# Kernel tuning notes

Hardware: AMD Instinct MI355X
Metric: run time of the kernel (lower is better)

Reference implementation:

```python
import jax, jax.numpy as jnp
import numpy as np
import math

D_MODEL, N_HEADS, D_HEAD = 1024, 16, 64
INIT_RANGE = 0.02
IGNORE = -100000.0


def setup_inputs() -> dict:
    key = jax.random.key(0)
    ks = jax.random.split(key, 5)
    x = jax.random.normal(ks[0], (2, 2048, D_MODEL), dtype=jnp.float32)
    W_Q = INIT_RANGE * jax.random.normal(ks[1], (N_HEADS, D_MODEL, D_HEAD), dtype=jnp.float32)
    W_K = INIT_RANGE * jax.random.normal(ks[2], (N_HEADS, D_MODEL, D_HEAD), dtype=jnp.float32)
    W_V = INIT_RANGE * jax.random.normal(ks[3], (N_HEADS, D_MODEL, D_HEAD), dtype=jnp.float32)
    # W_O is contracted as 'n_heads d_head d_model' in the original einsum
    W_O = INIT_RANGE * jax.random.normal(ks[4], (N_HEADS, D_HEAD, D_MODEL), dtype=jnp.float32)
    b_Q = jnp.zeros((N_HEADS, D_HEAD), dtype=jnp.float32)
    b_K = jnp.zeros((N_HEADS, D_HEAD), dtype=jnp.float32)
    b_V = jnp.zeros((N_HEADS, D_HEAD), dtype=jnp.float32)
    b_O = jnp.zeros((D_MODEL,), dtype=jnp.float32)
    return {"normalized_resid_pre": x, "W_Q": W_Q, "b_Q": b_Q, "W_K": W_K, "b_K": b_K,
            "W_V": W_V, "b_V": b_V, "W_O": W_O, "b_O": b_O}


def reference(normalized_resid_pre, W_Q, b_Q, W_K, b_K, W_V, b_V, W_O, b_O):
    x = normalized_resid_pre  # [b, s, d_model]
    q = jnp.einsum('bsd,hde->bshe', x, W_Q) + b_Q  # [b, s, h, d_head]
    k = jnp.einsum('bsd,hde->bshe', x, W_K) + b_K
    v = jnp.einsum('bsd,hde->bshe', x, W_V) + b_V
    scores = jnp.einsum('bqhe,bkhe->bhqk', q, k) / math.sqrt(D_HEAD)
    S = x.shape[1]
    causal = jnp.tril(jnp.ones((S, S), dtype=bool))  # True where allowed
    scores = jnp.where(causal, scores, IGNORE)
    pattern = jax.nn.softmax(scores, axis=-1)  # [b, h, q, k]
    z = jnp.einsum('bhqk,bkhe->bqhe', pattern, v)
    attn_out = jnp.einsum('bqhe,hed->bqd', z, W_O) + b_O
    return attn_out
```

## Files before the change

### kernel.cpp

```cpp
#include <hip/hip_runtime.h>
#include <cstdint>
#include <cstddef>

typedef unsigned short u16;
typedef __bf16 bf16x8 __attribute__((ext_vector_type(8)));
typedef _Float16 f16x4 __attribute__((ext_vector_type(4)));
typedef _Float16 f16x2 __attribute__((ext_vector_type(2)));
typedef float  f32x4  __attribute__((ext_vector_type(4)));
typedef unsigned short u16x8 __attribute__((ext_vector_type(8)));
typedef unsigned short u16x4 __attribute__((ext_vector_type(4)));

#define DM   1024
#define NH   16
#define DH   64
#define SS   2048
#define BSZ  4096
#define NQKV 3072
#define QSCALE 0.18033688011f

__device__ __forceinline__ u16 f2b(float f) {
  unsigned u = __builtin_bit_cast(unsigned, f);
  return (u16)((u + 0x7FFFu + ((u >> 16) & 1u)) >> 16);
}
__device__ __forceinline__ u16 f2h(float f) {
  _Float16 h = (_Float16)f;
  return __builtin_bit_cast(u16, h);
}

__device__ __forceinline__ void gl_lds16(const void* g, void* l) {
  __builtin_amdgcn_global_load_lds(
      (__attribute__((address_space(1))) void*)(void*)g,
      (__attribute__((address_space(3))) void*)l, 16, 0, 0);
}

__global__ __launch_bounds__(256) void prep_all_kernel(
    const float* __restrict__ x, u16* __restrict__ xb,
    const float* __restrict__ Wq, const float* __restrict__ Wk,
    const float* __restrict__ Wv, u16* __restrict__ wqkvt,
    const float* __restrict__ Wo, u16* __restrict__ wot) {
  __shared__ __align__(16) u16 Ts[64 * 72];
  int bid = blockIdx.x, t = threadIdx.x;
  if (bid < 2048) {
    int i = (bid * 256 + t) * 8;
    float4 a = *(const float4*)(x + i);
    float4 b = *(const float4*)(x + i + 4);
    u16x8 o;
    o[0] = f2b(a.x); o[1] = f2b(a.y); o[2] = f2b(a.z); o[3] = f2b(a.w);
    o[4] = f2b(b.x); o[5] = f2b(b.y); o[6] = f2b(b.z); o[7] = f2b(b.w);
    *(u16x8*)(xb + i) = o;
    return;
  }
  if (bid < 2816) {
    int idx = bid - 2048;
    int dt = idx & 15, sl = idx >> 4;
    int proj = sl >> 4, h = sl & 15;
    const float* W = (proj == 0) ? Wq : ((proj == 1) ? Wk : Wv);
    int d0 = dt * 64;
    {
      int ld = t >> 2;
      int ec = (t & 3) * 16;
      const float* src = W + ((size_t)h * DM + d0 + ld) * DH + ec;
      float4 v0 = *(const float4*)(src);
      float4 v1 = *(const float4*)(src + 4);
      float4 v2 = *(const float4*)(src + 8);
      float4 v3 = *(const float4*)(src + 12);
      float vv[16] = {v0.x, v0.y, v0.z, v0.w, v1.x, v1.y, v1.z, v1.w,
                      v2.x, v2.y, v2.z, v2.w, v3.x, v3.y, v3.z, v3.w};
#pragma unroll
      for (int i = 0; i < 16; i++) Ts[(ec + i) * 72 + ld] = f2b(vv[i]);
    }
    __syncthreads();
    {
      int le = t >> 2;
      int dc = (t & 3) * 16;
      int n = proj * DM + h * DH + le;
      u16* dst = wqkvt + (size_t)n * DM + d0 + dc;
      *(u16x8*)(dst)     = *(const u16x8*)&Ts[le * 72 + dc];
      *(u16x8*)(dst + 8) = *(const u16x8*)&Ts[le * 72 + dc + 8];
    }
    return;
  }
  {
    int idx = bid - 2816;
    int dt = idx & 15, h = idx >> 4;
    int d0 = dt * 64;
    {
      int le = t >> 2;
      int dc = (t & 3) * 16;
      const float* src = Wo + ((size_t)h * DH + le) * DM + d0 + dc;
      float4 v0 = *(const float4*)(src);
      float4 v1 = *(const float4*)(src + 4);
      float4 v2 = *(const float4*)(src + 8);
      float4 v3 = *(const float4*)(src + 12);
      float vv[16] = {v0.x, v0.y, v0.z, v0.w, v1.x, v1.y, v1.z, v1.w,
                      v2.x, v2.y, v2.z, v2.w, v3.x, v3.y, v3.z, v3.w};
#pragma unroll
      for (int i = 0; i < 16; i++) Ts[(dc + i) * 72 + le] = f2b(vv[i]);
    }
    __syncthreads();
    {
      int ld = t >> 2;
      int ec = (t & 3) * 16;
      u16* dst = wot + (size_t)(d0 + ld) * DM + h * DH + ec;
      *(u16x8*)(dst)     = *(const u16x8*)&Ts[ld * 72 + ec];
      *(u16x8*)(dst + 8) = *(const u16x8*)&Ts[ld * 72 + ec + 8];
    }
  }
}

__global__ __launch_bounds__(256) void gemm_qkv_kernel(
    const u16* __restrict__ A, const u16* __restrict__ Bt,
    u16* __restrict__ o_q, u16* __restrict__ o_k, u16* __restrict__ o_v,
    const float* __restrict__ c0, const float* __restrict__ c1,
    const float* __restrict__ c2) {
  const int K = DM;
  __shared__ __align__(16) u16 As[128 * 32];
  __shared__ __align__(16) u16 Bs[128 * 32];
  __shared__ __align__(16) u16 Cs[64 * 128];
  int t = threadIdx.x, w = t >> 6, l = t & 63;
  int lr = l & 15, lq = l >> 4;
  int m0 = blockIdx.x * 128, n0 = blockIdx.y * 128;
  int wr = w >> 1, wc = w & 1;
  f32x4 acc[4][4] = {};
  const u16* ga = A + (size_t)(m0 + (t >> 2)) * K + (t & 3) * 8;
  const u16* gb = Bt + (size_t)(n0 + (t >> 2)) * K + (t & 3) * 8;

  for (int k0 = 0; k0 < K; k0 += 32) {
    __syncthreads();
    gl_lds16(ga + k0,           &As[w * 512]);
    gl_lds16(ga + k0 + 64 * K,  &As[2048 + w * 512]);
    gl_lds16(gb + k0,           &Bs[w * 512]);
    gl_lds16(gb + k0 + 64 * K,  &Bs[2048 + w * 512]);
    __syncthreads();
    bf16x8 af[4], bfr[4];
#pragma unroll
    for (int i = 0; i < 4; i++)
      af[i] = *(const bf16x8*)&As[(wr * 64 + i * 16 + lr) * 32 + lq * 8];
#pragma unroll
    for (int j = 0; j < 4; j++)
      bfr[j] = *(const bf16x8*)&Bs[(wc * 64 + j * 16 + lr) * 32 + lq * 8];
#pragma unroll
    for (int i = 0; i < 4; i++)
#pragma unroll
      for (int j = 0; j < 4; j++)
        acc[i][j] = __builtin_amdgcn_mfma_f32_16x16x32_bf16(af[i], bfr[j], acc[i][j], 0, 0, 0);
  }

  int proj = n0 >> 10;
  int r0 = n0 & 1023;
  int h0 = r0 >> 6;
  const float* bp = (proj == 0) ? c0 : ((proj == 1) ? c1 : c2);

#pragma unroll
  for (int p = 0; p < 2; p++) {
    __syncthreads();
    if (wr == p) {
#pragma unroll
      for (int j = 0; j < 4; j++) {
        int nl = wc * 64 + j * 16 + lr;
        float bias = bp[r0 + nl];
#pragma unroll
        for (int i = 0; i < 4; i++) {
#pragma unroll
          for (int g = 0; g < 4; g++) {
            int ml = i * 16 + lq * 4 + g;
            float val = acc[i][j][g] + bias;
            if (proj == 0)      Cs[ml * 128 + nl] = f2b(val * QSCALE);
            else if (proj == 1) Cs[ml * 128 + nl] = f2b(val);
            else                Cs[nl * 64 + ml] = f2h(val);
          }
        }
      }
    }
    __syncthreads();
    int m_base = m0 + p * 64;
    if (proj < 2) {
      int ml = t >> 2, q4 = t & 3;
      int hh = q4 >> 1, e0 = (q4 & 1) * 32;
      int m = m_base + ml, b = m >> 11, s = m & 2047;
      int h = h0 + hh;
      u16* dst = (proj == 0 ? o_q : o_k) + ((size_t)(b * NH + h) * SS + s) * DH + e0;
      const u16* src = &Cs[ml * 128 + hh * 64 + e0];
      *(u16x8*)(dst)      = *(const u16x8*)(src);
      *(u16x8*)(dst + 8)  = *(const u16x8*)(src + 8);
      *(u16x8*)(dst + 16) = *(const u16x8*)(src + 16);
      *(u16x8*)(dst + 24) = *(const u16x8*)(src + 24);
    } else {
      int er = t >> 1, sh = t & 1;
      int hh = er >> 6, e = er & 63;
      int h = h0 + hh;
      int ms = m_base + sh * 32, b = ms >> 11, s = ms & 2047;
      u16* dst = o_v + ((size_t)(b * NH + h) * DH + e) * SS + s;
      const u16* src = &Cs[er * 64 + sh * 32];
      *(u16x8*)(dst)      = *(const u16x8*)(src);
      *(u16x8*)(dst + 8)  = *(const u16x8*)(src + 8);
      *(u16x8*)(dst + 16) = *(const u16x8*)(src + 16);
      *(u16x8*)(dst + 24) = *(const u16x8*)(src + 24);
    }
  }
}

__global__ __launch_bounds__(256) void gemm_o_kernel(
    const u16* __restrict__ A, const u16* __restrict__ Bt,
    const float* __restrict__ bo, float* __restrict__ fout) {
  const int K = DM;
  __shared__ __align__(16) u16 As[128 * 32];
  __shared__ __align__(16) u16 Bs[64 * 32];
  int t = threadIdx.x, w = t >> 6, l = t & 63;
  int lr = l & 15, lq = l >> 4;
  int m0 = blockIdx.x * 128, n0 = blockIdx.y * 64;
  f32x4 acc[2][4] = {};
  const u16* ga = A + (size_t)(m0 + (t >> 2)) * K + (t & 3) * 8;
  const u16* gb = Bt + (size_t)(n0 + (t >> 2)) * K + (t & 3) * 8;

  for (int k0 = 0; k0 < K; k0 += 32) {
    __syncthreads();
    gl_lds16(ga + k0,           &As[w * 512]);
    gl_lds16(ga + k0 + 64 * K,  &As[2048 + w * 512]);
    gl_lds16(gb + k0, &Bs[w * 512]);
    __syncthreads();
    bf16x8 af[2], bfr[4];
#pragma unroll
    for (int i = 0; i < 2; i++)
      af[i] = *(const bf16x8*)&As[(w * 32 + i * 16 + lr) * 32 + lq * 8];
#pragma unroll
    for (int j = 0; j < 4; j++)
      bfr[j] = *(const bf16x8*)&Bs[(j * 16 + lr) * 32 + lq * 8];
#pragma unroll
    for (int i = 0; i < 2; i++)
#pragma unroll
      for (int j = 0; j < 4; j++)
        acc[i][j] = __builtin_amdgcn_mfma_f32_16x16x32_bf16(af[i], bfr[j], acc[i][j], 0, 0, 0);
  }

  int mb = m0 + w * 32 + lq * 4;
  int nb = n0 + lr;
#pragma unroll
  for (int j = 0; j < 4; j++) {
    int n = nb + j * 16;
    float bias = bo[n];
#pragma unroll
    for (int i = 0; i < 2; i++) {
#pragma unroll
      for (int g = 0; g < 4; g++) {
        int m = mb + i * 16 + g;
        fout[(size_t)m * DM + n] = acc[i][j][g] + bias;
      }
    }
  }
}

__global__ __launch_bounds__(512) void attn_kernel(const u16* __restrict__ q_ws,
                                                   const u16* __restrict__ k_ws,
                                                   const u16* __restrict__ vt_ws,
                                                   u16* __restrict__ z_ws) {
  __shared__ __align__(16) u16 KsA[2][64 * 72], VsA[2][64 * 72];
  __shared__ __align__(16) u16 KsB[2][64 * 72], VsB[2][64 * 72];
  __shared__ float lbuf[2][64];

  int t = threadIdx.x;
  int g = t >> 8;
  int tl = t & 255;
  int w4 = tl >> 6;
  int l = t & 63;
  int lr = l & 15, lq = l >> 4;
  int srow = tl >> 3;
  int sc8 = (tl & 7) * 8;

  u16 (*Ks)[64 * 72] = g ? KsB : KsA;
  u16 (*Vs)[64 * 72] = g ? VsB : VsA;

  int bid = blockIdx.x;
  int xcd = bid & 7, idx = bid >> 3;
  int bh = xcd * 4 + (idx & 3);
  int j = idx >> 2;
  const u16* Qb = q_ws + (size_t)bh * SS * DH;
  const u16* Kb = k_ws + (size_t)bh * SS * DH;
  const u16* Vb = vt_ws + (size_t)bh * DH * SS;
  int b = bh >> 4, h16 = bh & 15;

  const f16x4 ones = {(_Float16)1.f, (_Float16)1.f, (_Float16)1.f, (_Float16)1.f};

  for (int half = 0; half < 2; half++) {
    int qt = half ? (31 - j) : j;
    int q0 = qt * 64;
    int nkt = qt + 1;
    int h = nkt >> 1;
    int cnt1 = nkt - h;
    int mycnt = g ? cnt1 : h;
    int base = g ? h : 0;

    int qrow = q0 + w4 * 16 + lr;
    bf16x8 qf0 = *(const bf16x8*)(Qb + (size_t)qrow * DH + lq * 8);
    bf16x8 qf1 = *(const bf16x8*)(Qb + (size_t)qrow * DH + 32 + lq * 8);

    f32x4 accO[4] = {};
    f32x4 accL = {};

    __syncthreads();
    if (mycnt > 0) {
      int k0 = base * 64;
      const u16* kg = Kb + (size_t)(k0 + srow) * DH + sc8;
      const u16* vg = Vb + (size_t)srow * SS + k0 + sc8;
      u16x8 r0 = *(const u16x8*)kg;
      u16x8 r1 = *(const u16x8*)(kg + 32 * DH);
      u16x8 r2 = *(const u16x8*)vg;
      u16x8 r3 = *(const u16x8*)(vg + 32 * SS);
      *(u16x8*)&Ks[0][srow * 72 + sc8] = r0;
      *(u16x8*)&Ks[0][(srow + 32) * 72 + sc8] = r1;
      *(u16x8*)&Vs[0][srow * 72 + sc8] = r2;
      *(u16x8*)&Vs[0][(srow + 32) * 72 + sc8] = r3;
    }

    for (int it = 0; it < cnt1; ++it) {
      __syncthreads();
      bool act = it < mycnt;
      int pb = it & 1;

      u16x8 r0, r1, r2, r3;
      bool have_next = (it + 1 < mycnt);
      if (have_next) {
        int k0n = (base + it + 1) * 64;
        const u16* kg = Kb + (size_t)(k0n + srow) * DH + sc8;
        const u16* vg = Vb + (size_t)srow * SS + k0n + sc8;
        r0 = *(const u16x8*)kg;
        r1 = *(const u16x8*)(kg + 32 * DH);
        r2 = *(const u16x8*)vg;
        r3 = *(const u16x8*)(vg + 32 * SS);
      }

      if (act) {
        f32x4 sc[4];
#pragma unroll
        for (int nt = 0; nt < 4; nt++) {
          bf16x8 kf0 = *(const bf16x8*)&Ks[pb][(nt * 16 + lr) * 72 + lq * 8];
          bf16x8 kf1 = *(const bf16x8*)&Ks[pb][(nt * 16 + lr) * 72 + 32 + lq * 8];
          f32x4 a = {0.f, 0.f, 0.f, 0.f};
          a = __builtin_amdgcn_mfma_f32_16x16x32_bf16(kf0, qf0, a, 0, 0, 0);
          a = __builtin_amdgcn_mfma_f32_16x16x32_bf16(kf1, qf1, a, 0, 0, 0);
          sc[nt] = a;
        }

        if (g == 1 && it == cnt1 - 1) {
          int k0 = (base + it) * 64;
          int gq = q0 + w4 * 16 + lr;
#pragma unroll
          for (int nt = 0; nt < 4; nt++) {
#pragma unroll
            for (int gg = 0; gg < 4; gg++) {
              int gk = k0 + nt * 16 + lq * 4 + gg;
              if (gk > gq) sc[nt][gg] = -1e30f;
            }
          }
        }

        f16x4 pf[4];
#pragma unroll
        for (int nt = 0; nt < 4; nt++) {
          float p0 = exp2f(sc[nt][0]);
          float p1 = exp2f(sc[nt][1]);
          float p2 = exp2f(sc[nt][2]);
          float p3 = exp2f(sc[nt][3]);
          f16x2 e0 = __builtin_bit_cast(f16x2, __builtin_amdgcn_cvt_pkrtz(p0, p1));
          f16x2 e1 = __builtin_bit_cast(f16x2, __builtin_amdgcn_cvt_pkrtz(p2, p3));
          pf[nt][0] = e0[0]; pf[nt][1] = e0[1];
          pf[nt][2] = e1[0]; pf[nt][3] = e1[1];
        }

#pragma unroll
        for (int ks = 0; ks < 4; ks++) {
          accL = __builtin_amdgcn_mfma_f32_16x16x16f16(ones, pf[ks], accL, 0, 0, 0);
#pragma unroll
          for (int et = 0; et < 4; et++) {
            f16x4 vf = *(const f16x4*)&Vs[pb][(et * 16 + lr) * 72 + ks * 16 + lq * 4];
            accO[et] = __builtin_amdgcn_mfma_f32_16x16x16f16(vf, pf[ks], accO[et], 0, 0, 0);
          }
        }
      }

      if (have_next) {
        int nb2 = (it + 1) & 1;
        *(u16x8*)&Ks[nb2][srow * 72 + sc8] = r0;
        *(u16x8*)&Ks[nb2][(srow + 32) * 72 + sc8] = r1;
        *(u16x8*)&Vs[nb2][srow * 72 + sc8] = r2;
        *(u16x8*)&Vs[nb2][(srow + 32) * 72 + sc8] = r3;
      }
    }

    __syncthreads();
    if (lq == 0) lbuf[g][w4 * 16 + lr] = accL[0];
    __syncthreads();
    float inv = 1.0f / (accL[0] + lbuf[1 - g][w4 * 16 + lr]);

    float* cbuf = (float*)VsB[1];
    int gq = q0 + w4 * 16 + lr;
    int crow = w4 * 16 + lr;
    u16* zrow = z_ws + ((size_t)(b * SS + gq)) * DM + h16 * DH;
#pragma unroll
    for (int c = 0; c < 2; c++) {
      if (g == 1) {
#pragma unroll
        for (int e2 = 0; e2 < 2; e2++) {
          int et = 2 * c + e2;
#pragma unroll
          for (int gg = 0; gg < 4; gg++)
            cbuf[crow * 32 + e2 * 16 + lq * 4 + gg] = accO[et][gg];
        }
      }
      __syncthreads();
      if (g == 0) {
#pragma unroll
        for (int e2 = 0; e2 < 2; e2++) {
          int et = 2 * c + e2;
          u16x4 o;
#pragma unroll
          for (int gg = 0; gg < 4; gg++) {
            float v = accO[et][gg] + cbuf[crow * 32 + e2 * 16 + lq * 4 + gg];
            o[gg] = f2b(v * inv);
          }
          *(u16x4*)(zrow + et * 16 + lq * 4) = o;
        }
      }
      __syncthreads();
    }
  }
}

extern "C" void kernel_launch(void* const* d_in, const int* in_sizes, int n_in,
                              void* d_out, int out_size, void* d_ws, size_t ws_size,
                              hipStream_t stream) {
  const float* x  = (const float*)d_in[0];
  const float* Wq = (const float*)d_in[1];
  const float* bq = (const float*)d_in[2];
  const float* Wk = (const float*)d_in[3];
  const float* bk = (const float*)d_in[4];
  const float* Wv = (const float*)d_in[5];
  const float* bv = (const float*)d_in[6];
  const float* Wo = (const float*)d_in[7];
  const float* bo = (const float*)d_in[8];
  float* out = (float*)d_out;

  char* ws = (char*)d_ws;
  const size_t MB = 1u << 20;
  u16* xb    = (u16*)(ws);
  u16* wqkvt = (u16*)(ws + 8 * MB);
  u16* wot   = (u16*)(ws + 14 * MB);
  u16* q_ws  = (u16*)(ws + 16 * MB);
  u16* k_ws  = (u16*)(ws + 24 * MB);
  u16* vt_ws = (u16*)(ws + 32 * MB);
  u16* z_ws  = (u16*)(ws + 40 * MB);

  prep_all_kernel<<<3072, 256, 0, stream>>>(x, xb, Wq, Wk, Wv, wqkvt, Wo, wot);

  gemm_qkv_kernel<<<dim3(BSZ / 128, NQKV / 128), 256, 0, stream>>>(
      xb, wqkvt, q_ws, k_ws, vt_ws, bq, bk, bv);

  attn_kernel<<<512, 512, 0, stream>>>(q_ws, k_ws, vt_ws, z_ws);

  gemm_o_kernel<<<dim3(BSZ / 128, DM / 64), 256, 0, stream>>>(z_ws, wot, bo, out);
}
```

Measured before the change: 191.0 us.

## Stage attention K/V tiles with direct global-to-LDS loads into swizzled buffers

Replaces the register-staged, double-buffered K/V tile prefetch with direct global-to-LDS loads (gl_lds16) into a single unpadded buffer per thread group. The buffer uses an XOR swizzle to avoid bank conflicts. This shrinks shared memory and drops the VGPR staging and explicit LDS stores, and launch bounds now request higher occupancy. In exchange, the loop now loads, syncs and computes in sequence with no software prefetch overlap, so the kernel relies on more resident waves to hide memory latency.

Result: slower. 205.9 us (+7.8%).

```diff
diff --git a/kernel.cpp b/kernel.cpp
--- a/kernel.cpp
+++ b/kernel.cpp
@@ -250,12 +250,12 @@
   }
 }
 
-__global__ __launch_bounds__(512) void attn_kernel(const u16* __restrict__ q_ws,
-                                                   const u16* __restrict__ k_ws,
-                                                   const u16* __restrict__ vt_ws,
-                                                   u16* __restrict__ z_ws) {
-  __shared__ __align__(16) u16 KsA[2][64 * 72], VsA[2][64 * 72];
-  __shared__ __align__(16) u16 KsB[2][64 * 72], VsB[2][64 * 72];
+__global__ __launch_bounds__(512, 8) void attn_kernel(const u16* __restrict__ q_ws,
+                                                      const u16* __restrict__ k_ws,
+                                                      const u16* __restrict__ vt_ws,
+                                                      u16* __restrict__ z_ws) {
+  __shared__ __align__(16) u16 Kt[2][64 * 64];
+  __shared__ __align__(16) u16 Vt[2][64 * 64];
   __shared__ float lbuf[2][64];
 
   int t = threadIdx.x;
@@ -264,11 +264,6 @@
   int w4 = tl >> 6;
   int l = t & 63;
   int lr = l & 15, lq = l >> 4;
-  int srow = tl >> 3;
-  int sc8 = (tl & 7) * 8;
-
-  u16 (*Ks)[64 * 72] = g ? KsB : KsA;
-  u16 (*Vs)[64 * 72] = g ? VsB : VsA;
 
   int bid = blockIdx.x;
   int xcd = bid & 7, idx = bid >> 3;
@@ -279,6 +274,26 @@
   const u16* Vb = vt_ws + (size_t)bh * DH * SS;
   int b = bh >> 4, h16 = bh & 15;
 
+  int sr = tl >> 3;
+  int gco = ((tl & 7) ^ (sr & 7)) * 8;
+  const u16* kgp = Kb + (size_t)sr * DH + gco;
+  const u16* vgp = Vb + (size_t)sr * SS + gco;
+  u16* kdst0 = &Kt[g][w4 * 512];
+  u16* kdst1 = &Kt[g][2048 + w4 * 512];
+  u16* vdst0 = &Vt[g][w4 * 512];
+  u16* vdst1 = &Vt[g][2048 + w4 * 512];
+
+  int rx = lr & 7;
+  int kc0 = (lq ^ rx) * 8;
+  int kc1 = ((lq + 4) ^ rx) * 8;
+  int rb[4];
+#pragma unroll
+  for (int i = 0; i < 4; i++) rb[i] = (i * 16 + lr) * 64;
+  int cx[4];
+#pragma unroll
+  for (int ks = 0; ks < 4; ks++)
+    cx[ks] = (((ks * 2 + (lq >> 1)) ^ rx) * 8) + (lq & 1) * 4;
+
   const f16x4 ones = {(_Float16)1.f, (_Float16)1.f, (_Float16)1.f, (_Float16)1.f};
 
   for (int half = 0; half < 2; half++) {
@@ -297,44 +312,24 @@
     f32x4 accO[4] = {};
     f32x4 accL = {};
 
-    __syncthreads();
-    if (mycnt > 0) {
-      int k0 = base * 64;
-      const u16* kg = Kb + (size_t)(k0 + srow) * DH + sc8;
-      const u16* vg = Vb + (size_t)srow * SS + k0 + sc8;
-      u16x8 r0 = *(const u16x8*)kg;
-      u16x8 r1 = *(const u16x8*)(kg + 32 * DH);
-      u16x8 r2 = *(const u16x8*)vg;
-      u16x8 r3 = *(const u16x8*)(vg + 32 * SS);
-      *(u16x8*)&Ks[0][srow * 72 + sc8] = r0;
-      *(u16x8*)&Ks[0][(srow + 32) * 72 + sc8] = r1;
-      *(u16x8*)&Vs[0][srow * 72 + sc8] = r2;
-      *(u16x8*)&Vs[0][(srow + 32) * 72 + sc8] = r3;
-    }
-
     for (int it = 0; it < cnt1; ++it) {
+      bool act = it < mycnt;
+      int k0 = (base + it) * 64;
       __syncthreads();
-      bool act = it < mycnt;
-      int pb = it & 1;
-
-      u16x8 r0, r1, r2, r3;
-      bool have_next = (it + 1 < mycnt);
-      if (have_next) {
-        int k0n = (base + it + 1) * 64;
-        const u16* kg = Kb + (size_t)(k0n + srow) * DH + sc8;
-        const u16* vg = Vb + (size_t)srow * SS + k0n + sc8;
-        r0 = *(const u16x8*)kg;
-        r1 = *(const u16x8*)(kg + 32 * DH);
-        r2 = *(const u16x8*)vg;
-        r3 = *(const u16x8*)(vg + 32 * SS);
-      }
+      if (act) {
+        gl_lds16(kgp + (size_t)k0 * DH, kdst0);
+        gl_lds16(kgp + (size_t)(k0 + 32) * DH, kdst1);
+        gl_lds16(vgp + k0, vdst0);
+        gl_lds16(vgp + 32 * SS + k0, vdst1);
+      }
+      __syncthreads();
 
       if (act) {
         f32x4 sc[4];
 #pragma unroll
         for (int nt = 0; nt < 4; nt++) {
-          bf16x8 kf0 = *(const bf16x8*)&Ks[pb][(nt * 16 + lr) * 72 + lq * 8];
-          bf16x8 kf1 = *(const bf16x8*)&Ks[pb][(nt * 16 + lr) * 72 + 32 + lq * 8];
+          bf16x8 kf0 = *(const bf16x8*)&Kt[g][rb[nt] + kc0];
+          bf16x8 kf1 = *(const bf16x8*)&Kt[g][rb[nt] + kc1];
           f32x4 a = {0.f, 0.f, 0.f, 0.f};
           a = __builtin_amdgcn_mfma_f32_16x16x32_bf16(kf0, qf0, a, 0, 0, 0);
           a = __builtin_amdgcn_mfma_f32_16x16x32_bf16(kf1, qf1, a, 0, 0, 0);
@@ -342,13 +337,13 @@
         }
 
         if (g == 1 && it == cnt1 - 1) {
-          int k0 = (base + it) * 64;
+          int k0d = (base + it) * 64;
           int gq = q0 + w4 * 16 + lr;
 #pragma unroll
           for (int nt = 0; nt < 4; nt++) {
 #pragma unroll
             for (int gg = 0; gg < 4; gg++) {
-              int gk = k0 + nt * 16 + lq * 4 + gg;
+              int gk = k0d + nt * 16 + lq * 4 + gg;
               if (gk > gq) sc[nt][gg] = -1e30f;
             }
           }
@@ -372,19 +367,11 @@
           accL = __builtin_amdgcn_mfma_f32_16x16x16f16(ones, pf[ks], accL, 0, 0, 0);
 #pragma unroll
           for (int et = 0; et < 4; et++) {
-            f16x4 vf = *(const f16x4*)&Vs[pb][(et * 16 + lr) * 72 + ks * 16 + lq * 4];
+            f16x4 vf = *(const f16x4*)&Vt[g][rb[et] + cx[ks]];
             accO[et] = __builtin_amdgcn_mfma_f32_16x16x16f16(vf, pf[ks], accO[et], 0, 0, 0);
           }
         }
       }
-
-      if (have_next) {
-        int nb2 = (it + 1) & 1;
-        *(u16x8*)&Ks[nb2][srow * 72 + sc8] = r0;
-        *(u16x8*)&Ks[nb2][(srow + 32) * 72 + sc8] = r1;
-        *(u16x8*)&Vs[nb2][srow * 72 + sc8] = r2;
-        *(u16x8*)&Vs[nb2][(srow + 32) * 72 + sc8] = r3;
-      }
     }
 
     __syncthreads();
@@ -392,7 +379,7 @@
     __syncthreads();
     float inv = 1.0f / (accL[0] + lbuf[1 - g][w4 * 16 + lr]);
 
-    float* cbuf = (float*)VsB[1];
+    float* cbuf = (float*)Vt[1];
     int gq = q0 + w4 * 16 + lr;
     int crow = w4 * 16 + lr;
     u16* zrow = z_ws + ((size_t)(b * SS + gq)) * DM + h16 * DH;
```
